# Kernel optimization log

Measured on AMD Instinct MI355X. Metric: run time of the kernel, lower is better.

Reference implementation:

```python
import jax, jax.numpy as jnp
import numpy as np

B, L, D, H = 8, 2048, 1024, 1024
BASE_LR, BASE_WD = 0.01, 0.9


def setup_inputs() -> dict:
    key = jax.random.key(0)
    ks = jax.random.split(key, 8)
    s = 1.0 / np.sqrt(D)
    return {
        "x": jax.random.normal(ks[0], (B, L, D), jnp.float32),
        "hidden": jax.random.normal(ks[1], (B, D, H), jnp.float32),
        "log_base_lr": jnp.array([np.log(BASE_LR)], jnp.float32),
        "w_lr": jax.random.normal(ks[2], (D, 1), jnp.float32) * s,
        "b_lr": jnp.zeros((1,), jnp.float32),
        "log_base_wd": jnp.array([np.log(BASE_WD)], jnp.float32),
        "w_wd": jax.random.normal(ks[3], (D, 1), jnp.float32) * s,
        "b_wd": jnp.zeros((1,), jnp.float32),
        "w_q": jax.random.normal(ks[4], (D, H), jnp.float32) * s,
        "b_q": jnp.zeros((H,), jnp.float32),
        "w_k": jax.random.normal(ks[5], (D, H), jnp.float32) * s,
        "b_k": jnp.zeros((H,), jnp.float32),
        "w_v": jax.random.normal(ks[6], (D, D), jnp.float32) * s,
        "b_v": jnp.zeros((D,), jnp.float32),
    }


def reference(x, hidden, log_base_lr, w_lr, b_lr, log_base_wd, w_wd, b_wd,
              w_q, b_q, w_k, b_k, w_v, b_v):
    batch, length, dim = x.shape
    W_prev = hidden  # [b, d, h]
    query = x @ w_q + b_q                     # [b, l, h]
    key = x @ w_k + b_k                       # [b, l, h]
    value = x @ w_v + b_v                     # [b, l, d]
    lr = jnp.exp(log_base_lr) * jax.nn.sigmoid((x @ w_lr + b_lr)[..., 0])  # [b, l]
    # log(1 - base_wd * sigmoid(.)) via log1p for stability; same math.
    log_wd = jnp.log1p(-jnp.exp(log_base_wd) * jax.nn.sigmoid((x @ w_wd + b_wd)[..., 0]))  # [b, l]
    wd_cross = jnp.exp(jnp.cumsum(log_wd, axis=1))  # [b, l]
    # inner-chunk decay: entry [b, m, l] = exp(sum_{j=m+1..l} log_wd[b, j]) for l >= m
    tri = jnp.triu(jnp.broadcast_to(log_wd[:, None, :], (batch, length, length)), k=1)
    wd_inner = jnp.triu(jnp.exp(jnp.cumsum(tri, axis=2)))  # [b, l, l]
    kq = jnp.einsum('bld,bmd->blm', key, query)            # [b, l, m]
    mask_kq = kq * wd_inner
    WpK_V = jnp.einsum('bdh,blh->bld', W_prev, key) - value  # [b, l, d]
    y_inner = -jnp.einsum('bld,bl,blm->bmd', WpK_V, lr, mask_kq)
    y_cross = jnp.einsum('bdh,blh,bl->bld', W_prev, query, wd_cross)
    y = y_inner + y_cross
    W_next_inner = -jnp.einsum('bld,bl,blh->bdh', WpK_V, lr * wd_inner[:, :, -1], key)
    W_next_cross = W_prev * wd_cross[:, -1][:, None, None]
    W_next = W_next_inner + W_next_cross
    return y, W_next
```

## Files before the change

### kernel.cpp

```cpp
#include <hip/hip_runtime.h>
#include <stdint.h>

#define BB 8
#define LL 2048
#define DD 1024
#define HH 1024
#define BL (BB*LL)

typedef __attribute__((ext_vector_type(8))) short short8;
typedef __attribute__((ext_vector_type(4))) float f32x4;

__device__ __forceinline__ unsigned short f2bf(float f) {
  unsigned int x = __float_as_uint(f);
  unsigned int r = (x + 0x7fffu + ((x >> 16) & 1u)) >> 16;
  return (unsigned short)r;
}
__device__ __forceinline__ float bf2f(unsigned short u) {
  return __uint_as_float(((unsigned int)u) << 16);
}

#define TM 128
#define TN 128
#define BK 64

struct __align__(16) Smem {
  unsigned short a[TM*BK];
  unsigned short b[TN*BK];
};

__device__ __forceinline__ void stage16(const unsigned short* g, unsigned short* l) {
  __builtin_amdgcn_global_load_lds((const __attribute__((address_space(1))) void*)g,
                                   (__attribute__((address_space(3))) void*)l,
                                   16, 0, 0);
}

__device__ __forceinline__ void gemm_core(const unsigned short* __restrict__ A, int lda,
                                          const unsigned short* __restrict__ B, int ldb,
                                          int m0, int n0, int ktiles,
                                          Smem* sm, f32x4 acc[4][4]) {
  const int tid  = threadIdx.x;
  const int lane = tid & 63;
  const int wave = tid >> 6;
  const int mw = (wave >> 1) * 64;
  const int nw = (wave & 1) * 64;
  const int srow = lane >> 3;
  const int scol = (((lane & 7) ^ srow) * 8);
  const int fk = (lane >> 4) * 8;
  const int fr = lane & 15;
  const int fx = fr & 7;
  for (int kt = 0; kt < ktiles; ++kt) {
    const int k0 = kt * BK;
#pragma unroll
    for (int r = 0; r < 4; ++r) {
      const int chunk = wave * 4 + r;
      const int row = chunk * 8 + srow;
      stage16(A + (size_t)(m0 + row) * lda + (k0 + scol), &sm->a[chunk * 512]);
      stage16(B + (size_t)(n0 + row) * ldb + (k0 + scol), &sm->b[chunk * 512]);
    }
    __syncthreads();
#pragma unroll
    for (int kk = 0; kk < BK; kk += 32) {
      const int kc = ((((kk + fk) >> 3) ^ fx) << 3);
      short8 af[4], bfv[4];
#pragma unroll
      for (int i = 0; i < 4; ++i)
        af[i] = *(const short8*)&sm->a[(mw + i*16 + fr) * BK + kc];
#pragma unroll
      for (int j = 0; j < 4; ++j)
        bfv[j] = *(const short8*)&sm->b[(nw + j*16 + fr) * BK + kc];
#pragma unroll
      for (int i = 0; i < 4; ++i)
#pragma unroll
        for (int j = 0; j < 4; ++j)
          acc[i][j] = __builtin_amdgcn_mfma_f32_16x16x32_bf16(af[i], bfv[j], acc[i][j], 0, 0, 0);
    }
    __syncthreads();
  }
}

__device__ __forceinline__ void acc_init(f32x4 acc[4][4]) {
#pragma unroll
  for (int i = 0; i < 4; ++i)
#pragma unroll
    for (int j = 0; j < 4; ++j)
      acc[i][j] = (f32x4){0.f, 0.f, 0.f, 0.f};
}

template <typename F>
__device__ __forceinline__ void epilogue_loop(const f32x4 acc[4][4], F body) {
  const int lane_ = threadIdx.x & 63;
  const int wave_ = threadIdx.x >> 6;
  const int mw_ = (wave_ >> 1) * 64, nw_ = (wave_ & 1) * 64;
#pragma unroll
  for (int mi = 0; mi < 4; ++mi)
#pragma unroll
    for (int ni = 0; ni < 4; ++ni)
#pragma unroll
      for (int j = 0; j < 4; ++j) {
        const int rr = mw_ + mi * 16 + ((lane_ >> 4) << 2) + j;
        const int cc = nw_ + ni * 16 + (lane_ & 15);
        body(rr, cc, acc[mi][ni][j]);
      }
}

__device__ __forceinline__ void xcd_map_u(int x, int i, int& bb, int& mt, int& nt) {
  bb = i >> 4;
  const int i16 = i & 15;
  const int sr = x >> 1, sc = x & 1;
  mt = 4 * (i16 & 3) + sr;
  nt = 4 * sc + (i16 >> 2);
}


__global__ void k_prep_x(const float* __restrict__ x, const float* __restrict__ wlr,
                         const float* __restrict__ wwd, unsigned short* __restrict__ xb,
                         float* __restrict__ lrlog, float* __restrict__ wdlog) {
  const int wave = threadIdx.x >> 6, lane = threadIdx.x & 63;
  const int row = blockIdx.x * 4 + wave;
  const float* xr = x + (size_t)row * DD;
  float s1 = 0.f, s2 = 0.f;
#pragma unroll
  for (int ch = 0; ch < 4; ++ch) {
    const int col = ch * 256 + lane * 4;
    float4 v = *(const float4*)(xr + col);
    float4 a = *(const float4*)(wlr + col);
    float4 b = *(const float4*)(wwd + col);
    s1 += v.x*a.x + v.y*a.y + v.z*a.z + v.w*a.w;
    s2 += v.x*b.x + v.y*b.y + v.z*b.z + v.w*b.w;
    uint2 u;
    u.x = (unsigned)f2bf(v.x) | ((unsigned)f2bf(v.y) << 16);
    u.y = (unsigned)f2bf(v.z) | ((unsigned)f2bf(v.w) << 16);
    *(uint2*)(xb + (size_t)row * DD + col) = u;
  }
#pragma unroll
  for (int off = 32; off > 0; off >>= 1) {
    s1 += __shfl_down(s1, off);
    s2 += __shfl_down(s2, off);
  }
  if (lane == 0) { lrlog[row] = s1; wdlog[row] = s2; }
}

__global__ void k_prep_w(const float* __restrict__ wq, const float* __restrict__ wk,
                         const float* __restrict__ wv, unsigned short* __restrict__ wqt,
                         unsigned short* __restrict__ wkt, unsigned short* __restrict__ wvtn,
                         unsigned short* __restrict__ wkr) {
  const int idx = blockIdx.x * 256 + threadIdx.x;
  if (blockIdx.z == 3) { wkr[idx] = f2bf(wk[idx]); return; }
  const int k = idx >> 10, n = idx & 1023;
  const float* src = (blockIdx.z == 0) ? wq : (blockIdx.z == 1) ? wk : wv;
  unsigned short* dst = (blockIdx.z == 0) ? wqt : (blockIdx.z == 1) ? wkt : wvtn;
  float v = src[(size_t)k * 1024 + n];
  if (blockIdx.z == 2) v = -v;
  dst[(size_t)n * 1024 + k] = f2bf(v);
}

__global__ void k_prep_h(const float* __restrict__ hid, unsigned short* __restrict__ wpb) {
  const size_t i = ((size_t)blockIdx.x * 256 + threadIdx.x) * 4;
  float4 v = *(const float4*)(hid + i);
  uint2 u;
  u.x = (unsigned)f2bf(v.x) | ((unsigned)f2bf(v.y) << 16);
  u.y = (unsigned)f2bf(v.z) | ((unsigned)f2bf(v.w) << 16);
  *(uint2*)(wpb + i) = u;
}

__global__ void k_bias2(const unsigned short* __restrict__ wpb, const float* __restrict__ bk,
                        const float* __restrict__ bv, float* __restrict__ bias2) {
  const int wave = threadIdx.x >> 6, lane = threadIdx.x & 63;
  const int row = blockIdx.x * 4 + wave;
  const unsigned short* wr = wpb + (size_t)row * HH;
  float s = 0.f;
#pragma unroll
  for (int ch = 0; ch < 4; ++ch) {
    const int col = ch * 256 + lane * 4;
    float4 a = *(const float4*)(bk + col);
    ushort4 u = *(const ushort4*)(wr + col);
    s += a.x * bf2f(u.x) + a.y * bf2f(u.y) + a.z * bf2f(u.z) + a.w * bf2f(u.w);
  }
#pragma unroll
  for (int off = 32; off > 0; off >>= 1) s += __shfl_down(s, off);
  if (lane == 0) bias2[row] = s - bv[row & 1023];
}

__global__ void k_scan(const float* __restrict__ lrlog, const float* __restrict__ wdlog,
                       const float* __restrict__ lbl, const float* __restrict__ blr,
                       const float* __restrict__ lbw, const float* __restrict__ bwd,
                       float* __restrict__ lr, float* __restrict__ c,
                       float* __restrict__ s, float* __restrict__ ecl) {
  const int b = blockIdx.x, t = threadIdx.x;
  __shared__ float sums[256];
  const float elr = expf(lbl[0]);
  const float ewd = expf(lbw[0]);
  const float blr0 = blr[0], bwd0 = bwd[0];
  float lw[8];
  const float* wb = wdlog + (size_t)b * LL + t * 8;
  float tot = 0.f;
#pragma unroll
  for (int i = 0; i < 8; ++i) {
    float z = wb[i] + bwd0;
    float sig = 1.f / (1.f + expf(-z));
    tot += log1pf(-ewd * sig);
    lw[i] = tot;
  }
  sums[t] = tot;
  __syncthreads();
  for (int off = 1; off < 256; off <<= 1) {
    float v = (t >= off) ? sums[t - off] : 0.f;
    __syncthreads();
    sums[t] += v;
    __syncthreads();
  }
  const float prev = (t > 0) ? sums[t - 1] : 0.f;
  const float ctot = sums[255];
  const float* lb = lrlog + (size_t)b * LL + t * 8;
#pragma unroll
  for (int i = 0; i < 8; ++i) {
    const int idx = b * LL + t * 8 + i;
    const float ci = prev + lw[i];
    c[idx] = ci;
    float zl = lb[i] + blr0;
    float lri = elr / (1.f + expf(-zl));
    lr[idx] = lri;
    s[idx] = lri * expf(ctot - ci);
  }
  if (t == 0) ecl[b] = expf(ctot);
}


__global__ __launch_bounds__(256) void k_gemm_m2(const unsigned short* __restrict__ wpb,
    const unsigned short* __restrict__ wkr, const unsigned short* __restrict__ wvtn,
    unsigned short* __restrict__ w2t) {
  const int b = blockIdx.z, mt = blockIdx.y, nt = blockIdx.x;
  __shared__ Smem sm;
  f32x4 acc[4][4]; acc_init(acc);
  gemm_core(wpb + (size_t)b * DD * HH, HH, wkr, HH, mt * TM, nt * TN, HH / BK, &sm, acc);
  epilogue_loop(acc, [&](int rr, int cc, float av) {
    const int d = mt * TM + rr, j = nt * TN + cc;
    const size_t gi = (size_t)d * DD + j;
    w2t[(size_t)b * DD * DD + gi] = f2bf(av + bf2f(wvtn[gi]));
  });
}

__global__ __launch_bounds__(256) void k_gemm_q(const unsigned short* __restrict__ xb,
    const unsigned short* __restrict__ wt, const float* __restrict__ bias,
    const float* __restrict__ c, unsigned short* __restrict__ outb,
    unsigned short* __restrict__ q2b) {
  int bb, mt, nt; xcd_map_u(blockIdx.x, blockIdx.y, bb, mt, nt);
  const int m0 = (bb * 16 + mt) * TM, n0 = nt * TN;
  __shared__ Smem sm;
  f32x4 acc[4][4]; acc_init(acc);
  gemm_core(xb, DD, wt, DD, m0, n0, DD / BK, &sm, acc);
  epilogue_loop(acc, [&](int rr, int cc, float av) {
    const int row = m0 + rr, col = n0 + cc;
    const float v = av + bias[col];
    outb[(size_t)row * HH + col] = f2bf(v);
    q2b[(size_t)row * HH + col] = f2bf(v * __expf(c[row]));
  });
}

__global__ __launch_bounds__(256) void k_gemm_k(const unsigned short* __restrict__ xb,
    const unsigned short* __restrict__ wt, const float* __restrict__ bias,
    const float* __restrict__ s, unsigned short* __restrict__ kb,
    unsigned short* __restrict__ k2t) {
  int bb, mt, nt; xcd_map_u(blockIdx.x, blockIdx.y, bb, mt, nt);
  const int m0 = (bb * 16 + mt) * TM, n0 = nt * TN;
  __shared__ Smem sm;
  f32x4 acc[4][4]; acc_init(acc);
  gemm_core(xb, DD, wt, DD, m0, n0, DD / BK, &sm, acc);
  const int lane = threadIdx.x & 63, wave = threadIdx.x >> 6;
  const int mw = (wave >> 1) * 64, nw = (wave & 1) * 64;
#pragma unroll
  for (int mi = 0; mi < 4; ++mi)
#pragma unroll
    for (int ni = 0; ni < 4; ++ni) {
      const int col = n0 + nw + ni*16 + (lane & 15);
      const float bias_c = bias[col];
      const int row0 = m0 + mw + mi*16 + ((lane >> 4) << 2);
      const int b = row0 >> 11, ml0 = row0 & 2047;
      unsigned short tmp[4];
#pragma unroll
      for (int j = 0; j < 4; ++j) {
        float v = acc[mi][ni][j] + bias_c;
        kb[(size_t)(row0 + j) * HH + col] = f2bf(v);
        tmp[j] = f2bf(v * s[row0 + j]);
      }
      uint2 u;
      u.x = (unsigned)tmp[0] | ((unsigned)tmp[1] << 16);
      u.y = (unsigned)tmp[2] | ((unsigned)tmp[3] << 16);
      *(uint2*)&k2t[((size_t)b * HH + col) * LL + ml0] = u;
    }
}

__global__ __launch_bounds__(256) void k_gemm_u(const unsigned short* __restrict__ xb,
    const unsigned short* __restrict__ w2t, const float* __restrict__ bias2,
    unsigned short* __restrict__ ut) {
  int bb, mt, nt; xcd_map_u(blockIdx.x, blockIdx.y, bb, mt, nt);
  const int m0 = (bb * 16 + mt) * TM, n0 = nt * TN;
  const int b = bb;
  __shared__ Smem sm;
  f32x4 acc[4][4]; acc_init(acc);
  gemm_core(xb, DD, w2t + (size_t)b * DD * DD, DD, m0, n0, DD / BK, &sm, acc);
  const int lane = threadIdx.x & 63, wave = threadIdx.x >> 6;
  const int mw = (wave >> 1) * 64, nw = (wave & 1) * 64;
#pragma unroll
  for (int mi = 0; mi < 4; ++mi)
#pragma unroll
    for (int ni = 0; ni < 4; ++ni) {
      const int col = n0 + nw + ni*16 + (lane & 15);
      const float b2c = bias2[b * DD + col];
      const int row0 = m0 + mw + mi*16 + ((lane >> 4) << 2);
      const int ml0 = row0 & 2047;
      unsigned short tmp[4];
#pragma unroll
      for (int j = 0; j < 4; ++j) tmp[j] = f2bf(acc[mi][ni][j] + b2c);
      uint2 u;
      u.x = (unsigned)tmp[0] | ((unsigned)tmp[1] << 16);
      u.y = (unsigned)tmp[2] | ((unsigned)tmp[3] << 16);
      *(uint2*)&ut[((size_t)b * DD + col) * LL + ml0] = u;
    }
}

__global__ __launch_bounds__(256) void k_gemm_p(const unsigned short* __restrict__ qb,
    const unsigned short* __restrict__ kb, const float* __restrict__ lr,
    const float* __restrict__ c, unsigned short* __restrict__ pb) {
  const int b = blockIdx.z;
  const int i = blockIdx.x;
  const int t = (i & 7) * 17 + (i >> 3);
  int mt = (int)((sqrtf(8.0f * (float)t + 1.0f) - 1.0f) * 0.5f);
  while ((mt + 1) * (mt + 2) / 2 <= t) ++mt;
  while (mt * (mt + 1) / 2 > t) --mt;
  const int nt = t - mt * (mt + 1) / 2;
  __shared__ Smem sm;
  f32x4 acc[4][4]; acc_init(acc);
  const int base = b * LL;
  const int m0g = base + mt * TM, n0g = base + nt * TN;
  gemm_core(qb, HH, kb, HH, m0g, n0g, HH / BK, &sm, acc);

  const int lane = threadIdx.x & 63, wave = threadIdx.x >> 6;
  const int mw = (wave >> 1) * 64, nw = (wave & 1) * 64;
  if (nt != mt) {
    const float cref = c[base + mt * TM];
    float er[4][4], fc[4];
#pragma unroll
    for (int mi = 0; mi < 4; ++mi)
#pragma unroll
      for (int j = 0; j < 4; ++j) {
        const int m = mt * TM + mw + mi*16 + ((lane >> 4) << 2) + j;
        er[mi][j] = __expf(c[base + m] - cref);
      }
#pragma unroll
    for (int ni = 0; ni < 4; ++ni) {
      const int l = nt * TN + nw + ni*16 + (lane & 15);
      fc[ni] = lr[base + l] * __expf(cref - c[base + l]);
    }
#pragma unroll
    for (int mi = 0; mi < 4; ++mi)
#pragma unroll
      for (int ni = 0; ni < 4; ++ni) {
        const int l = nt * TN + nw + ni*16 + (lane & 15);
        const int row0 = mt * TM + mw + mi*16 + ((lane >> 4) << 2);
#pragma unroll
        for (int j = 0; j < 4; ++j) {
          const float v = -acc[mi][ni][j] * er[mi][j] * fc[ni];
          pb[((size_t)base + row0 + j) * LL + l] = f2bf(v);
        }
      }
  } else {
    epilogue_loop(acc, [&](int rr, int cc, float av) {
      const int m = mt * TM + rr, l = nt * TN + cc;
      float v = 0.f;
      if (l <= m) v = -av * lr[base + l] * __expf(c[base + m] - c[base + l]);
      pb[((size_t)base + m) * LL + l] = f2bf(v);
    });
  }
}

__global__ __launch_bounds__(256) void k_gemm_y(const unsigned short* __restrict__ pb,
    const unsigned short* __restrict__ ut, const unsigned short* __restrict__ q2b,
    const unsigned short* __restrict__ wpb, float* __restrict__ out) {
  const int b = blockIdx.z;
  const int x = blockIdx.x, i16 = blockIdx.y;
  const int sr = x >> 1, sc = x & 1;
  const int lm = i16 & 3, ln = i16 >> 2;
  const int mt = (lm == 0) ? (15 - sr) : (lm == 1) ? (8 + sr)
               : (lm == 2) ? (7 - sr)  : sr;
  const int nt = 4 * sc + ln;
  __shared__ Smem sm;
  f32x4 acc[4][4]; acc_init(acc);
  gemm_core(pb + (size_t)b * LL * LL, LL, ut + (size_t)b * DD * LL, LL,
            mt * TM, nt * TN, (mt + 1) * 2, &sm, acc);
  gemm_core(q2b, HH, wpb + (size_t)b * DD * HH, HH,
            b * LL + mt * TM, nt * TN, HH / BK, &sm, acc);
  epilogue_loop(acc, [&](int rr, int cc, float av) {
    const int m = mt * TM + rr, d = nt * TN + cc;
    out[((size_t)b * LL + m) * DD + d] = av;
  });
}

__global__ __launch_bounds__(256) void k_gemm_wn(const unsigned short* __restrict__ ut,
    const unsigned short* __restrict__ k2t, const float* __restrict__ hid,
    const float* __restrict__ ecl, float* __restrict__ out2) {
  const int b = blockIdx.z;
  const int x = blockIdx.x, i8 = blockIdx.y;
  const int sr = x >> 2, sc = x & 3;
  const int mt = 4 * sr + (i8 & 3);
  const int nt = 2 * sc + (i8 >> 2);
  __shared__ Smem sm;
  f32x4 acc[4][4]; acc_init(acc);
  gemm_core(ut + (size_t)b * DD * LL, LL, k2t + (size_t)b * HH * LL, LL,
            mt * TM, nt * TN, LL / BK, &sm, acc);
  epilogue_loop(acc, [&](int rr, int cc, float av) {
    const int d = mt * TM + rr, h = nt * TN + cc;
    const size_t gi = ((size_t)b * DD + d) * HH + h;
    out2[gi] = -av + ecl[b] * hid[gi];
  });
}


extern "C" void kernel_launch(void* const* d_in, const int* in_sizes, int n_in,
                              void* d_out, int out_size, void* d_ws, size_t ws_size,
                              hipStream_t stream) {
  (void)in_sizes; (void)n_in; (void)out_size; (void)ws_size;
  const float* x   = (const float*)d_in[0];
  const float* hid = (const float*)d_in[1];
  const float* lbl = (const float*)d_in[2];
  const float* wlr = (const float*)d_in[3];
  const float* blr = (const float*)d_in[4];
  const float* lbw = (const float*)d_in[5];
  const float* wwd = (const float*)d_in[6];
  const float* bwd = (const float*)d_in[7];
  const float* wq  = (const float*)d_in[8];
  const float* bq  = (const float*)d_in[9];
  const float* wk  = (const float*)d_in[10];
  const float* bk  = (const float*)d_in[11];
  const float* wv  = (const float*)d_in[12];
  const float* bv  = (const float*)d_in[13];
  float* out = (float*)d_out;

  char* w = (char*)d_ws;
  constexpr size_t SZ_XB  = (size_t)BL * DD * 2;
  constexpr size_t SZ_QB  = (size_t)BL * HH * 2;
  constexpr size_t SZ_KB  = (size_t)BL * HH * 2;
  constexpr size_t SZ_K2T = (size_t)BB * HH * LL * 2;
  constexpr size_t SZ_UT  = (size_t)BB * DD * LL * 2;
  constexpr size_t SZ_PB  = (size_t)BB * LL * LL * 2;
  constexpr size_t SZ_WT  = (size_t)DD * HH * 2;
  constexpr size_t SZ_WPB = (size_t)BB * DD * HH * 2;
  constexpr size_t SZ_V16 = (size_t)BL * 4;

  size_t off = 0;
  unsigned short* xb   = (unsigned short*)(w + off); off += SZ_XB;
  unsigned short* qb   = (unsigned short*)(w + off); off += SZ_QB;
  unsigned short* kb   = (unsigned short*)(w + off); off += SZ_KB;
  unsigned short* k2t  = (unsigned short*)(w + off); off += SZ_K2T;
  unsigned short* ut   = (unsigned short*)(w + off); off += SZ_UT;
  unsigned short* pb   = (unsigned short*)(w + off); off += SZ_PB;
  unsigned short* wqt  = (unsigned short*)(w + off); off += SZ_WT;
  unsigned short* wkt  = (unsigned short*)(w + off); off += SZ_WT;
  unsigned short* wvtn = (unsigned short*)(w + off); off += SZ_WT;
  unsigned short* wpb  = (unsigned short*)(w + off); off += SZ_WPB;
  float* lrlog = (float*)(w + off); off += SZ_V16;
  float* wdlog = (float*)(w + off); off += SZ_V16;
  float* lr    = (float*)(w + off); off += SZ_V16;
  float* c     = (float*)(w + off); off += SZ_V16;
  float* s     = (float*)(w + off); off += SZ_V16;
  float* ecl   = (float*)(w + off); off += 256;
  float* bias2 = (float*)(w + off); off += (size_t)BB * DD * 4;

  unsigned short* w2t = pb;
  unsigned short* wkr = pb + (size_t)BB * DD * DD;

  unsigned short* q2b = (unsigned short*)(out + (size_t)BL * DD);
  float* out2 = out + (size_t)BL * DD;

  k_prep_x<<<dim3(BL / 4), 256, 0, stream>>>(x, wlr, wwd, xb, lrlog, wdlog);
  k_prep_w<<<dim3(4096, 1, 4), 256, 0, stream>>>(wq, wk, wv, wqt, wkt, wvtn, wkr);
  k_prep_h<<<dim3((unsigned)((size_t)BB * DD * HH / 1024)), 256, 0, stream>>>(hid, wpb);
  k_scan<<<dim3(BB), 256, 0, stream>>>(lrlog, wdlog, lbl, blr, lbw, bwd, lr, c, s, ecl);
  k_bias2<<<dim3(BB * DD / 4), 256, 0, stream>>>(wpb, bk, bv, bias2);

  k_gemm_m2<<<dim3(DD / TN, DD / TM, BB), 256, 0, stream>>>(wpb, wkr, wvtn, w2t);
  k_gemm_q<<<dim3(8, BL / TM / 16 * 16), 256, 0, stream>>>(xb, wqt, bq, c, qb, q2b);
  k_gemm_k<<<dim3(8, BL / TM), 256, 0, stream>>>(xb, wkt, bk, s, kb, k2t);
  k_gemm_u<<<dim3(8, BL / TM), 256, 0, stream>>>(xb, w2t, bias2, ut);
  k_gemm_p<<<dim3(136, 1, BB), 256, 0, stream>>>(qb, kb, lr, c, pb);
  k_gemm_y<<<dim3(8, 16, BB), 256, 0, stream>>>(pb, ut, q2b, wpb, out);
  k_gemm_wn<<<dim3(8, 8, BB), 256, 0, stream>>>(ut, k2t, hid, ecl, out2);
}
```

Baseline: 665.5 us.

## Switch GEMMs to larger 512-thread tiles with double-buffered LDS staging

Adds a new templated GEMM core that uses 8 waves per block, larger output tiles (128x256 or 256x256) and double-buffered LDS, so global loads for the next K tile overlap the MFMA work on the current one. Six GEMM kernels are moved onto it with new grid mappings. The y kernel fuses its two K-loops into one pipelined loop. The aim is more data reuse per tile and hidden load latency, at the cost of more LDS and registers per block, fewer blocks per grid, and a changed block-to-XCD ordering.

```diff
diff --git a/kernel.cpp b/kernel.cpp
--- a/kernel.cpp
+++ b/kernel.cpp
@@ -19,6 +19,12 @@
   return __uint_as_float(((unsigned int)u) << 16);
 }
 
+__device__ __forceinline__ void stage16(const unsigned short* g, unsigned short* l) {
+  __builtin_amdgcn_global_load_lds((const __attribute__((address_space(1))) void*)g,
+                                   (__attribute__((address_space(3))) void*)l,
+                                   16, 0, 0);
+}
+
 #define TM 128
 #define TN 128
 #define BK 64
@@ -27,12 +33,6 @@
   unsigned short a[TM*BK];
   unsigned short b[TN*BK];
 };
-
-__device__ __forceinline__ void stage16(const unsigned short* g, unsigned short* l) {
-  __builtin_amdgcn_global_load_lds((const __attribute__((address_space(1))) void*)g,
-                                   (__attribute__((address_space(3))) void*)l,
-                                   16, 0, 0);
-}
 
 __device__ __forceinline__ void gemm_core(const unsigned short* __restrict__ A, int lda,
                                           const unsigned short* __restrict__ B, int ldb,
@@ -103,12 +103,99 @@
       }
 }
 
-__device__ __forceinline__ void xcd_map_u(int x, int i, int& bb, int& mt, int& nt) {
-  bb = i >> 4;
-  const int i16 = i & 15;
-  const int sr = x >> 1, sc = x & 1;
-  mt = 4 * (i16 & 3) + sr;
-  nt = 4 * sc + (i16 >> 2);
+template<int MI>
+struct __align__(16) Smem2 {
+  unsigned short a[2][MI*2048];
+  unsigned short b[2][16384];
+};
+
+template<int MI>
+__device__ __forceinline__ void acc_init2(f32x4 (&acc)[MI][4]) {
+#pragma unroll
+  for (int i = 0; i < MI; ++i)
+#pragma unroll
+    for (int j = 0; j < 4; ++j)
+      acc[i][j] = (f32x4){0.f, 0.f, 0.f, 0.f};
+}
+
+template<int MI, class FA, class FB>
+__device__ __forceinline__ void gemm2_core(FA srcA, FB srcB, int NK,
+                                           Smem2<MI>* sm, f32x4 (&acc)[MI][4]) {
+  const int lane = threadIdx.x & 63;
+  const int wave = threadIdx.x >> 6;
+  const int srow = lane >> 3;
+  const int scol = ((lane & 7) ^ srow) * 8;
+  constexpr int APW = MI / 2;
+  const int fk = (lane >> 4) * 8;
+  const int fr = lane & 15;
+  const int fx = fr & 7;
+  const int mwr = (wave >> 2) * (MI * 16);
+  const int nwr = (wave & 3) * 64;
+
+  auto STAGE = [&](int p, int kt) {
+#pragma unroll
+    for (int r = 0; r < APW; ++r) {
+      const int chunk = wave * APW + r;
+      stage16(srcA(chunk * 8 + srow, kt) + scol, &sm->a[p][chunk * 512]);
+    }
+#pragma unroll
+    for (int r = 0; r < 4; ++r) {
+      const int chunk = wave * 4 + r;
+      stage16(srcB(chunk * 8 + srow, kt) + scol, &sm->b[p][chunk * 512]);
+    }
+  };
+  auto COMPUTE = [&](int p) {
+    const unsigned short* pa  = sm->a[p];
+    const unsigned short* pbp = sm->b[p];
+#pragma unroll
+    for (int kk = 0; kk < 64; kk += 32) {
+      const int kc = ((((kk + fk) >> 3) ^ fx) << 3);
+      short8 af[MI], bfv[4];
+#pragma unroll
+      for (int i = 0; i < MI; ++i)
+        af[i] = *(const short8*)&pa[(mwr + i*16 + fr) * 64 + kc];
+#pragma unroll
+      for (int j = 0; j < 4; ++j)
+        bfv[j] = *(const short8*)&pbp[(nwr + j*16 + fr) * 64 + kc];
+#pragma unroll
+      for (int i = 0; i < MI; ++i)
+#pragma unroll
+        for (int j = 0; j < 4; ++j)
+          acc[i][j] = __builtin_amdgcn_mfma_f32_16x16x32_bf16(af[i], bfv[j], acc[i][j], 0, 0, 0);
+    }
+  };
+
+  STAGE(0, 0);
+  asm volatile("s_waitcnt vmcnt(0)" ::: "memory");
+  __builtin_amdgcn_s_barrier();
+  __builtin_amdgcn_sched_barrier(0);
+  int cur = 0;
+  for (int kt = 0; kt < NK - 1; ++kt) {
+    STAGE(cur ^ 1, kt + 1);
+    COMPUTE(cur);
+    asm volatile("s_waitcnt vmcnt(0)" ::: "memory");
+    __builtin_amdgcn_s_barrier();
+    __builtin_amdgcn_sched_barrier(0);
+    cur ^= 1;
+  }
+  COMPUTE(cur);
+}
+
+template<int MI, typename F>
+__device__ __forceinline__ void epi2(const f32x4 (&acc)[MI][4], F body) {
+  const int lane = threadIdx.x & 63;
+  const int wave = threadIdx.x >> 6;
+  const int mwr = (wave >> 2) * (MI * 16), nwr = (wave & 3) * 64;
+#pragma unroll
+  for (int i = 0; i < MI; ++i)
+#pragma unroll
+    for (int j = 0; j < 4; ++j)
+#pragma unroll
+      for (int jj = 0; jj < 4; ++jj) {
+        const int rr = mwr + i * 16 + ((lane >> 4) << 2) + jj;
+        const int cc = nwr + j * 16 + (lane & 15);
+        body(rr, cc, acc[i][j][jj]);
+      }
 }
 
 
@@ -226,30 +313,38 @@
 }
 
 
-__global__ __launch_bounds__(256) void k_gemm_m2(const unsigned short* __restrict__ wpb,
+__global__ __launch_bounds__(512, 2) void k2_gemm_m2(const unsigned short* __restrict__ wpb,
     const unsigned short* __restrict__ wkr, const unsigned short* __restrict__ wvtn,
     unsigned short* __restrict__ w2t) {
-  const int b = blockIdx.z, mt = blockIdx.y, nt = blockIdx.x;
-  __shared__ Smem sm;
-  f32x4 acc[4][4]; acc_init(acc);
-  gemm_core(wpb + (size_t)b * DD * HH, HH, wkr, HH, mt * TM, nt * TN, HH / BK, &sm, acc);
-  epilogue_loop(acc, [&](int rr, int cc, float av) {
-    const int d = mt * TM + rr, j = nt * TN + cc;
-    const size_t gi = (size_t)d * DD + j;
+  __shared__ Smem2<4> sm;
+  const int b = blockIdx.x;
+  const int mt = blockIdx.y & 7, nt = blockIdx.y >> 3;
+  const int m0 = mt * 128, n0 = nt * 256;
+  f32x4 acc[4][4]; acc_init2<4>(acc);
+  gemm2_core<4>(
+    [&](int r, int kt) { return wpb + (size_t)b * DD * HH + (size_t)(m0 + r) * HH + kt * 64; },
+    [&](int r, int kt) { return wkr + (size_t)(n0 + r) * HH + kt * 64; },
+    HH / 64, &sm, acc);
+  epi2<4>(acc, [&](int rr, int cc, float av) {
+    const size_t gi = (size_t)(m0 + rr) * DD + (n0 + cc);
     w2t[(size_t)b * DD * DD + gi] = f2bf(av + bf2f(wvtn[gi]));
   });
 }
 
-__global__ __launch_bounds__(256) void k_gemm_q(const unsigned short* __restrict__ xb,
+__global__ __launch_bounds__(512, 2) void k2_gemm_q(const unsigned short* __restrict__ xb,
     const unsigned short* __restrict__ wt, const float* __restrict__ bias,
     const float* __restrict__ c, unsigned short* __restrict__ outb,
     unsigned short* __restrict__ q2b) {
-  int bb, mt, nt; xcd_map_u(blockIdx.x, blockIdx.y, bb, mt, nt);
-  const int m0 = (bb * 16 + mt) * TM, n0 = nt * TN;
-  __shared__ Smem sm;
-  f32x4 acc[4][4]; acc_init(acc);
-  gemm_core(xb, DD, wt, DD, m0, n0, DD / BK, &sm, acc);
-  epilogue_loop(acc, [&](int rr, int cc, float av) {
+  __shared__ Smem2<8> sm;
+  const int mt = blockIdx.x * 8 + (blockIdx.y & 7);
+  const int nt = blockIdx.y >> 3;
+  const int m0 = mt * 256, n0 = nt * 256;
+  f32x4 acc[8][4]; acc_init2<8>(acc);
+  gemm2_core<8>(
+    [&](int r, int kt) { return xb + (size_t)(m0 + r) * DD + kt * 64; },
+    [&](int r, int kt) { return wt + (size_t)(n0 + r) * DD + kt * 64; },
+    DD / 64, &sm, acc);
+  epi2<8>(acc, [&](int rr, int cc, float av) {
     const int row = m0 + rr, col = n0 + cc;
     const float v = av + bias[col];
     outb[(size_t)row * HH + col] = f2bf(v);
@@ -257,31 +352,35 @@
   });
 }
 
-__global__ __launch_bounds__(256) void k_gemm_k(const unsigned short* __restrict__ xb,
+__global__ __launch_bounds__(512, 2) void k2_gemm_k(const unsigned short* __restrict__ xb,
     const unsigned short* __restrict__ wt, const float* __restrict__ bias,
     const float* __restrict__ s, unsigned short* __restrict__ kb,
     unsigned short* __restrict__ k2t) {
-  int bb, mt, nt; xcd_map_u(blockIdx.x, blockIdx.y, bb, mt, nt);
-  const int m0 = (bb * 16 + mt) * TM, n0 = nt * TN;
-  __shared__ Smem sm;
-  f32x4 acc[4][4]; acc_init(acc);
-  gemm_core(xb, DD, wt, DD, m0, n0, DD / BK, &sm, acc);
+  __shared__ Smem2<8> sm;
+  const int mt = blockIdx.x * 8 + (blockIdx.y & 7);
+  const int nt = blockIdx.y >> 3;
+  const int m0 = mt * 256, n0 = nt * 256;
+  f32x4 acc[8][4]; acc_init2<8>(acc);
+  gemm2_core<8>(
+    [&](int r, int kt) { return xb + (size_t)(m0 + r) * DD + kt * 64; },
+    [&](int r, int kt) { return wt + (size_t)(n0 + r) * DD + kt * 64; },
+    DD / 64, &sm, acc);
   const int lane = threadIdx.x & 63, wave = threadIdx.x >> 6;
-  const int mw = (wave >> 1) * 64, nw = (wave & 1) * 64;
-#pragma unroll
-  for (int mi = 0; mi < 4; ++mi)
-#pragma unroll
-    for (int ni = 0; ni < 4; ++ni) {
-      const int col = n0 + nw + ni*16 + (lane & 15);
+  const int mwr = (wave >> 2) * 128, nwr = (wave & 3) * 64;
+#pragma unroll
+  for (int i = 0; i < 8; ++i)
+#pragma unroll
+    for (int j = 0; j < 4; ++j) {
+      const int col = n0 + nwr + j*16 + (lane & 15);
       const float bias_c = bias[col];
-      const int row0 = m0 + mw + mi*16 + ((lane >> 4) << 2);
+      const int row0 = m0 + mwr + i*16 + ((lane >> 4) << 2);
       const int b = row0 >> 11, ml0 = row0 & 2047;
       unsigned short tmp[4];
 #pragma unroll
-      for (int j = 0; j < 4; ++j) {
-        float v = acc[mi][ni][j] + bias_c;
-        kb[(size_t)(row0 + j) * HH + col] = f2bf(v);
-        tmp[j] = f2bf(v * s[row0 + j]);
+      for (int jj = 0; jj < 4; ++jj) {
+        float v = acc[i][j][jj] + bias_c;
+        kb[(size_t)(row0 + jj) * HH + col] = f2bf(v);
+        tmp[jj] = f2bf(v * s[row0 + jj]);
       }
       uint2 u;
       u.x = (unsigned)tmp[0] | ((unsigned)tmp[1] << 16);
@@ -290,28 +389,32 @@
     }
 }
 
-__global__ __launch_bounds__(256) void k_gemm_u(const unsigned short* __restrict__ xb,
+__global__ __launch_bounds__(512, 2) void k2_gemm_u(const unsigned short* __restrict__ xb,
     const unsigned short* __restrict__ w2t, const float* __restrict__ bias2,
     unsigned short* __restrict__ ut) {
-  int bb, mt, nt; xcd_map_u(blockIdx.x, blockIdx.y, bb, mt, nt);
-  const int m0 = (bb * 16 + mt) * TM, n0 = nt * TN;
-  const int b = bb;
-  __shared__ Smem sm;
-  f32x4 acc[4][4]; acc_init(acc);
-  gemm_core(xb, DD, w2t + (size_t)b * DD * DD, DD, m0, n0, DD / BK, &sm, acc);
+  __shared__ Smem2<8> sm;
+  const int b = blockIdx.x;
+  const int mt = blockIdx.x * 8 + (blockIdx.y & 7);
+  const int nt = blockIdx.y >> 3;
+  const int m0 = mt * 256, n0 = nt * 256;
+  f32x4 acc[8][4]; acc_init2<8>(acc);
+  gemm2_core<8>(
+    [&](int r, int kt) { return xb + (size_t)(m0 + r) * DD + kt * 64; },
+    [&](int r, int kt) { return w2t + (size_t)b * DD * DD + (size_t)(n0 + r) * DD + kt * 64; },
+    DD / 64, &sm, acc);
   const int lane = threadIdx.x & 63, wave = threadIdx.x >> 6;
-  const int mw = (wave >> 1) * 64, nw = (wave & 1) * 64;
-#pragma unroll
-  for (int mi = 0; mi < 4; ++mi)
-#pragma unroll
-    for (int ni = 0; ni < 4; ++ni) {
-      const int col = n0 + nw + ni*16 + (lane & 15);
+  const int mwr = (wave >> 2) * 128, nwr = (wave & 3) * 64;
+#pragma unroll
+  for (int i = 0; i < 8; ++i)
+#pragma unroll
+    for (int j = 0; j < 4; ++j) {
+      const int col = n0 + nwr + j*16 + (lane & 15);
       const float b2c = bias2[b * DD + col];
-      const int row0 = m0 + mw + mi*16 + ((lane >> 4) << 2);
+      const int row0 = m0 + mwr + i*16 + ((lane >> 4) << 2);
       const int ml0 = row0 & 2047;
       unsigned short tmp[4];
 #pragma unroll
-      for (int j = 0; j < 4; ++j) tmp[j] = f2bf(acc[mi][ni][j] + b2c);
+      for (int jj = 0; jj < 4; ++jj) tmp[jj] = f2bf(acc[i][j][jj] + b2c);
       uint2 u;
       u.x = (unsigned)tmp[0] | ((unsigned)tmp[1] << 16);
       u.y = (unsigned)tmp[2] | ((unsigned)tmp[3] << 16);
@@ -374,44 +477,47 @@
   }
 }
 
-__global__ __launch_bounds__(256) void k_gemm_y(const unsigned short* __restrict__ pb,
+__global__ __launch_bounds__(512, 2) void k2_gemm_y(const unsigned short* __restrict__ pb,
     const unsigned short* __restrict__ ut, const unsigned short* __restrict__ q2b,
     const unsigned short* __restrict__ wpb, float* __restrict__ out) {
-  const int b = blockIdx.z;
-  const int x = blockIdx.x, i16 = blockIdx.y;
-  const int sr = x >> 1, sc = x & 1;
-  const int lm = i16 & 3, ln = i16 >> 2;
-  const int mt = (lm == 0) ? (15 - sr) : (lm == 1) ? (8 + sr)
-               : (lm == 2) ? (7 - sr)  : sr;
-  const int nt = 4 * sc + ln;
-  __shared__ Smem sm;
-  f32x4 acc[4][4]; acc_init(acc);
-  gemm_core(pb + (size_t)b * LL * LL, LL, ut + (size_t)b * DD * LL, LL,
-            mt * TM, nt * TN, (mt + 1) * 2, &sm, acc);
-  gemm_core(q2b, HH, wpb + (size_t)b * DD * HH, HH,
-            b * LL + mt * TM, nt * TN, HH / BK, &sm, acc);
-  epilogue_loop(acc, [&](int rr, int cc, float av) {
-    const int m = mt * TM + rr, d = nt * TN + cc;
-    out[((size_t)b * LL + m) * DD + d] = av;
+  __shared__ Smem2<4> sm;
+  const int b = blockIdx.x;
+  const int mt = 15 - (blockIdx.y & 15);
+  const int nt = blockIdx.y >> 4;
+  const int m0 = mt * 128, n0 = nt * 256;
+  const int NK1 = (mt + 1) * 2;
+  f32x4 acc[4][4]; acc_init2<4>(acc);
+  gemm2_core<4>(
+    [&](int r, int kt) {
+      return (kt < NK1) ? pb + (size_t)b * LL * LL + (size_t)(m0 + r) * LL + kt * 64
+                        : q2b + ((size_t)b * LL + m0 + r) * HH + (kt - NK1) * 64;
+    },
+    [&](int r, int kt) {
+      return (kt < NK1) ? ut + (size_t)b * DD * LL + (size_t)(n0 + r) * LL + kt * 64
+                        : wpb + (size_t)b * DD * HH + (size_t)(n0 + r) * HH + (kt - NK1) * 64;
+    },
+    NK1 + 16, &sm, acc);
+  epi2<4>(acc, [&](int rr, int cc, float av) {
+    out[((size_t)b * LL + m0 + rr) * DD + (n0 + cc)] = av;
   });
 }
 
-__global__ __launch_bounds__(256) void k_gemm_wn(const unsigned short* __restrict__ ut,
+__global__ __launch_bounds__(512, 2) void k2_gemm_wn(const unsigned short* __restrict__ ut,
     const unsigned short* __restrict__ k2t, const float* __restrict__ hid,
     const float* __restrict__ ecl, float* __restrict__ out2) {
-  const int b = blockIdx.z;
-  const int x = blockIdx.x, i8 = blockIdx.y;
-  const int sr = x >> 2, sc = x & 3;
-  const int mt = 4 * sr + (i8 & 3);
-  const int nt = 2 * sc + (i8 >> 2);
-  __shared__ Smem sm;
-  f32x4 acc[4][4]; acc_init(acc);
-  gemm_core(ut + (size_t)b * DD * LL, LL, k2t + (size_t)b * HH * LL, LL,
-            mt * TM, nt * TN, LL / BK, &sm, acc);
-  epilogue_loop(acc, [&](int rr, int cc, float av) {
-    const int d = mt * TM + rr, h = nt * TN + cc;
-    const size_t gi = ((size_t)b * DD + d) * HH + h;
-    out2[gi] = -av + ecl[b] * hid[gi];
+  __shared__ Smem2<4> sm;
+  const int b = blockIdx.x;
+  const int mt = blockIdx.y & 7, nt = blockIdx.y >> 3;
+  const int m0 = mt * 128, n0 = nt * 256;
+  f32x4 acc[4][4]; acc_init2<4>(acc);
+  gemm2_core<4>(
+    [&](int r, int kt) { return ut + (size_t)b * DD * LL + (size_t)(m0 + r) * LL + kt * 64; },
+    [&](int r, int kt) { return k2t + (size_t)b * HH * LL + (size_t)(n0 + r) * LL + kt * 64; },
+    LL / 64, &sm, acc);
+  const float eclb = ecl[b];
+  epi2<4>(acc, [&](int rr, int cc, float av) {
+    const size_t gi = ((size_t)b * DD + (m0 + rr)) * HH + (n0 + cc);
+    out2[gi] = -av + eclb * hid[gi];
   });
 }
 
@@ -478,11 +584,11 @@
   k_scan<<<dim3(BB), 256, 0, stream>>>(lrlog, wdlog, lbl, blr, lbw, bwd, lr, c, s, ecl);
   k_bias2<<<dim3(BB * DD / 4), 256, 0, stream>>>(wpb, bk, bv, bias2);
 
-  k_gemm_m2<<<dim3(DD / TN, DD / TM, BB), 256, 0, stream>>>(wpb, wkr, wvtn, w2t);
-  k_gemm_q<<<dim3(8, BL / TM / 16 * 16), 256, 0, stream>>>(xb, wqt, bq, c, qb, q2b);
-  k_gemm_k<<<dim3(8, BL / TM), 256, 0, stream>>>(xb, wkt, bk, s, kb, k2t);
-  k_gemm_u<<<dim3(8, BL / TM), 256, 0, stream>>>(xb, w2t, bias2, ut);
+  k2_gemm_m2<<<dim3(8, 32), 512, 0, stream>>>(wpb, wkr, wvtn, w2t);
+  k2_gemm_q<<<dim3(8, 32), 512, 0, stream>>>(xb, wqt, bq, c, qb, q2b);
+  k2_gemm_k<<<dim3(8, 32), 512, 0, stream>>>(xb, wkt, bk, s, kb, k2t);
+  k2_gemm_u<<<dim3(8, 32), 512, 0, stream>>>(xb, w2t, bias2, ut);
   k_gemm_p<<<dim3(136, 1, BB), 256, 0, stream>>>(qb, kb, lr, c, pb);
-  k_gemm_y<<<dim3(8, 16, BB), 256, 0, stream>>>(pb, ut, q2b, wpb, out);
-  k_gemm_wn<<<dim3(8, 8, BB), 256, 0, stream>>>(ut, k2t, hid, ecl, out2);
-}
+  k2_gemm_y<<<dim3(8, 64), 512, 0, stream>>>(pb, ut, q2b, wpb, out);
+  k2_gemm_wn<<<dim3(8, 32), 512, 0, stream>>>(ut, k2t, hid, ecl, out2);
+}
```

New measurement: 628.4 us. 1.06x faster.
